# Performance work log

Hardware: AMD Instinct MI355X
Metric: run time of the kernel (lower is better)

The kernel has to match this reference:

```python
import jax, jax.numpy as jnp
import numpy as np

B, H, S, D = 8, 16, 1024, 128


def setup_inputs() -> dict:
    key = jax.random.key(0)
    kq, kk, kv = jax.random.split(key, 3)
    queries = jax.random.normal(kq, (B, H, S, D), dtype=jnp.float32)
    keys = jax.random.normal(kk, (B, H, S, D), dtype=jnp.float32)
    values = jax.random.normal(kv, (B, H, S, D), dtype=jnp.float32)
    # learnable per-element scale over the full score tensor, init 'ones'
    scale = jnp.ones((B, H, S, S), dtype=jnp.float32)
    return {"queries": queries, "keys": keys, "values": values, "scale": scale}


def reference(queries, keys, values, scale):
    # scores: [B,H,Sq,Sk] = Q K^T
    scores = jnp.einsum("bhqd,bhkd->bhqk", queries, keys)
    # custom learnable scaling: scores / sqrt(scale[0]) * scale
    # scale[0] has shape [H,Sq,Sk] and broadcasts over the batch dim
    scores = scores / jnp.sqrt(scale[0]) * scale
    # masked_softmax with attention_mask=None -> plain softmax over keys axis
    attn = jax.nn.softmax(scores, axis=-1)
    # dropout is identity (rate 0 / eval mode)
    out = jnp.einsum("bhqk,bhkd->bhqd", attn, values)
    return out
```

## Files before the change

### kernel.cpp

```cpp
#include <hip/hip_runtime.h>
#include <math.h>

#define NB 8
#define NH 16
#define NS 1024
#define ND 128

#define BN 32
#define NT (NS / BN)
#define TILE_SH (BN * ND)
#define PSTR 40

typedef float    f32x4 __attribute__((ext_vector_type(4)));
typedef _Float16 f16x8 __attribute__((ext_vector_type(8)));
typedef _Float16 f16x4 __attribute__((ext_vector_type(4)));

#define MFMAH(a, b, c) __builtin_amdgcn_mfma_f32_16x16x32_f16(a, b, c, 0, 0, 0)

__device__ __forceinline__ void gload16(const void* g, void* l) {
  __builtin_amdgcn_global_load_lds(
      (const __attribute__((address_space(1))) void*)g,
      (__attribute__((address_space(3))) void*)l, 16, 0, 0);
}

__global__ void prep_kv(const float* __restrict__ K, short* __restrict__ Kimg,
                        const float* __restrict__ V, short* __restrict__ Vimg) {
  __shared__ _Float16 tbuf[BN * 132];
  const int x = blockIdx.x;
  const int tid = threadIdx.x;
  if (x < 4096) {
    const int t = x & 31, bh = x >> 5;
    const float* Kt = K + ((size_t)bh * NS + t * BN) * ND;
    short* img = Kimg + ((size_t)bh * NT + t) * TILE_SH;
#pragma unroll
    for (int i = 0; i < 4; ++i) {
      int f = tid + i * 256;
      int key = f >> 5, d4 = (f & 31) << 2;
      float4 v = *(const float4*)(Kt + (size_t)key * ND + d4);
      f16x4 hv = {(_Float16)v.x, (_Float16)v.y, (_Float16)v.z, (_Float16)v.w};
      int gp = (d4 >> 3) ^ (key & 15);
      *(f16x4*)(img + key * 128 + gp * 8 + (d4 & 7)) = hv;
    }
  } else {
    const int p = x - 4096;
    const int t = p & 31, bh = p >> 5;
    const float* Vt = V + ((size_t)bh * NS + t * BN) * ND;
#pragma unroll
    for (int i = 0; i < 4; ++i) {
      int f = tid + i * 256;
      int key = f >> 5, d4 = (f & 31) << 2;
      float4 v = *(const float4*)(Vt + (size_t)key * ND + d4);
      *(f16x4*)&tbuf[key * 132 + d4] =
          (f16x4){(_Float16)v.x, (_Float16)v.y, (_Float16)v.z, (_Float16)v.w};
    }
    __syncthreads();
    short* img = Vimg + ((size_t)bh * NT + t) * TILE_SH;
#pragma unroll
    for (int i = 0; i < 2; ++i) {
      int u = tid + i * 256;
      int d = u >> 2, k8 = u & 3;
      f16x8 o;
#pragma unroll
      for (int e = 0; e < 8; ++e) o[e] = tbuf[(k8 * 8 + e) * 132 + d];
      *(f16x8*)(img + d * BN + ((k8 ^ ((d >> 1) & 3)) * 8)) = o;
    }
  }
}


#define ISSUE(T, B)                                              \
  do {                                                           \
    const short* kg_ = Kb + (T) * TILE_SH + tid * 8;             \
    const short* vg_ = Vb + (T) * TILE_SH + tid * 8;             \
    gload16(kg_, &Ks[B][tid * 8]);                               \
    gload16(kg_ + 2048, &Ks[B][tid * 8 + 2048]);                 \
    gload16(vg_, &Vs[B][tid * 8]);                               \
    gload16(vg_ + 2048, &Vs[B][tid * 8 + 2048]);                 \
  } while (0)

#define LOADS(SV, S0, T)                                                             \
  do {                                                                               \
    _Pragma("unroll") for (int nf = 0; nf < 2; ++nf)                                 \
        _Pragma("unroll") for (int m0 = 0; m0 < 2; ++m0) {                           \
      size_t off_ = (size_t)(q0 + nf * 16 + c) * NS + (T) * BN + m0 * 16 + quad * 4; \
      SV[nf][m0] = *(const f32x4*)(sclb + off_);                                     \
      S0[nf][m0] = *(const f32x4*)(sc0b + off_);                                     \
    }                                                                                \
  } while (0)

#define TILE_STEP(BUF, SCV, SC0)                                                     \
  do {                                                                               \
    f32x4 S_[2][2];                                                                  \
    _Pragma("unroll") for (int nf = 0; nf < 2; ++nf)                                 \
        _Pragma("unroll") for (int m0 = 0; m0 < 2; ++m0)                             \
            S_[nf][m0] = (f32x4){0.f, 0.f, 0.f, 0.f};                                \
    __builtin_amdgcn_s_setprio(1);                                                   \
    _Pragma("unroll") for (int m0 = 0; m0 < 2; ++m0) {                               \
      _Pragma("unroll") for (int kb = 0; kb < 4; ++kb) {                             \
        const f16x8 a_ = *(const f16x8*)&Ks[BUF][(m0 * 16 + c) * 128 +               \
                                                 (((kb << 2) | quad) ^ c) * 8];      \
        S_[0][m0] = MFMAH(a_, qf[0][kb], S_[0][m0]);                                 \
        S_[1][m0] = MFMAH(a_, qf[1][kb], S_[1][m0]);                                 \
      }                                                                              \
    }                                                                                \
    __builtin_amdgcn_s_setprio(0);                                                   \
    float al2_[2];                                                                   \
    int skipall_ = 1;                                                                \
    _Pragma("unroll") for (int nf = 0; nf < 2; ++nf) {                               \
      float sv[8];                                                                   \
      _Pragma("unroll") for (int m0 = 0; m0 < 2; ++m0)                               \
          _Pragma("unroll") for (int r = 0; r < 4; ++r) {                            \
        float e_ = SCV[nf][m0][r] * rsqrtf(SC0[nf][m0][r]);                          \
        sv[m0 * 4 + r] = S_[nf][m0][r] * e_;                                         \
      }                                                                              \
      float tm = sv[0];                                                              \
      _Pragma("unroll") for (int i = 1; i < 8; ++i) tm = fmaxf(tm, sv[i]);           \
      tm = fmaxf(tm, __shfl_xor(tm, 16));                                            \
      tm = fmaxf(tm, __shfl_xor(tm, 32));                                            \
      float mn, al;                                                                  \
      if (__all(tm <= m_[nf])) {                         \
        mn = m_[nf]; al = 1.f;                                                       \
      } else {                                                                       \
        mn = fmaxf(m_[nf], tm);                                                      \
        al = __expf(m_[nf] - mn);                                                    \
        m_[nf] = mn;                                                                 \
        skipall_ = 0;                                                                \
      }                                                                              \
      al2_[nf] = al;                                                                 \
      float ps = 0.f;                                                                \
      _Float16 pb[8];                                                                \
      _Pragma("unroll") for (int i = 0; i < 8; ++i) {                                \
        float p_ = __expf(sv[i] - mn);                                               \
        ps += p_;                                                                    \
        pb[i] = (_Float16)p_;                                                        \
      }                                                                              \
      ps += __shfl_xor(ps, 16);                                                      \
      ps += __shfl_xor(ps, 32);                                                      \
      ls_[nf] = ls_[nf] * al + ps;                                                   \
      _Float16* pr_ = &Ps[(size_t)(w * 32 + nf * 16 + c) * PSTR];                    \
      *(f16x4*)(pr_ + quad * 4)      = (f16x4){pb[0], pb[1], pb[2], pb[3]};          \
      *(f16x4*)(pr_ + 16 + quad * 4) = (f16x4){pb[4], pb[5], pb[6], pb[7]};          \
    }                                                                                \
    if (!skipall_) {                                                                 \
      _Pragma("unroll") for (int pf = 0; pf < 2; ++pf) {                             \
        float ar_[4];                                                                \
        _Pragma("unroll") for (int r = 0; r < 4; ++r)                                \
            ar_[r] = __shfl(al2_[pf], quad * 4 + r);                                 \
        _Pragma("unroll") for (int n0 = 0; n0 < 8; ++n0)                             \
            _Pragma("unroll") for (int r = 0; r < 4; ++r) O[pf][n0][r] *= ar_[r];    \
      }                                                                              \
    }                                                                                \
    const f16x8 pf0_ = *(const f16x8*)&Ps[(size_t)(w * 32 + c) * PSTR + quad * 8];   \
    const f16x8 pf1_ =                                                               \
        *(const f16x8*)&Ps[(size_t)(w * 32 + 16 + c) * PSTR + quad * 8];             \
    __builtin_amdgcn_s_setprio(1);                                                   \
    _Pragma("unroll") for (int n0 = 0; n0 < 8; ++n0) {                               \
      const f16x8 b_ = *(const f16x8*)&Vs[BUF][(n0 * 16 + c) * 32 +                  \
                                              (quad ^ ((c >> 1) & 3)) * 8];          \
      O[0][n0] = MFMAH(pf0_, b_, O[0][n0]);                                          \
      O[1][n0] = MFMAH(pf1_, b_, O[1][n0]);                                          \
    }                                                                                \
    __builtin_amdgcn_s_setprio(0);                                                   \
  } while (0)

__launch_bounds__(256, 2)
__global__ void attn_f16(const float* __restrict__ Q, const short* __restrict__ Kimg,
                         const short* __restrict__ Vimg, const float* __restrict__ scale,
                         float* __restrict__ out) {
  __shared__ short Ks[2][TILE_SH];
  __shared__ short Vs[2][TILE_SH];
  __shared__ _Float16 Ps[128 * PSTR];

  const int tid = threadIdx.x;
  const int w = tid >> 6, l = tid & 63;
  const int quad = l >> 4, c = l & 15;

  const int x = blockIdx.x;
  const int bh = ((x >> 6) << 3) | (x & 7);
  const int qblk = (x >> 3) & 7;
  const int q0 = qblk * 128 + w * 32;

  const short* Kb = Kimg + (size_t)bh * (NT * TILE_SH);
  const short* Vb = Vimg + (size_t)bh * (NT * TILE_SH);
  const float* sclb = scale + ((size_t)bh << 20);
  const float* sc0b = scale + ((size_t)(bh & 15) << 20);

  f16x8 qf[2][4];
  f32x4 sclvA[2][2], sc0vA[2][2], sclvB[2][2], sc0vB[2][2];
  {
    const float* Qb = Q + ((size_t)bh * NS + q0) * ND;
    float4 qa[2][4][2];
#pragma unroll
    for (int nf = 0; nf < 2; ++nf)
#pragma unroll
      for (int kb = 0; kb < 4; ++kb) {
        const float* p = Qb + (size_t)(nf * 16 + c) * ND + kb * 32 + quad * 8;
        qa[nf][kb][0] = *(const float4*)p;
        qa[nf][kb][1] = *(const float4*)(p + 4);
      }
    ISSUE(0, 0);
    LOADS(sclvA, sc0vA, 0);
#pragma unroll
    for (int nf = 0; nf < 2; ++nf)
#pragma unroll
      for (int kb = 0; kb < 4; ++kb) {
        float4 a = qa[nf][kb][0], b = qa[nf][kb][1];
        qf[nf][kb] = (f16x8){(_Float16)a.x, (_Float16)a.y, (_Float16)a.z, (_Float16)a.w,
                             (_Float16)b.x, (_Float16)b.y, (_Float16)b.z, (_Float16)b.w};
      }
  }

  float m_[2] = {-INFINITY, -INFINITY}, ls_[2] = {0.f, 0.f};
  f32x4 O[2][8];
#pragma unroll
  for (int pf = 0; pf < 2; ++pf)
#pragma unroll
    for (int n0 = 0; n0 < 8; ++n0) O[pf][n0] = (f32x4){0.f, 0.f, 0.f, 0.f};

#pragma unroll 1
  for (int kt = 0; kt < NT; kt += 2) {
    __syncthreads();
    ISSUE(kt + 1, 1);
    LOADS(sclvB, sc0vB, kt + 1);
    TILE_STEP(0, sclvA, sc0vA);
    __syncthreads();
    if (kt + 2 < NT) {
      ISSUE(kt + 2, 0);
      LOADS(sclvA, sc0vA, kt + 2);
    }
    TILE_STEP(1, sclvB, sc0vB);
  }

  float* ob = out + ((size_t)bh * NS + q0) * ND;
#pragma unroll
  for (int pf = 0; pf < 2; ++pf)
#pragma unroll
    for (int r = 0; r < 4; ++r) {
      float lv = __shfl(ls_[pf], quad * 4 + r);
      float inv = 1.0f / lv;
      int row = pf * 16 + quad * 4 + r;
#pragma unroll
      for (int n0 = 0; n0 < 8; ++n0)
        ob[(size_t)row * ND + n0 * 16 + c] = O[pf][n0][r] * inv;
    }
}

#define TQ 16
#define TK 64
#define PITCH 129
__launch_bounds__(256, 2)
__global__ void attn_fp32(const float* __restrict__ Q, const float* __restrict__ K,
                          const float* __restrict__ V, const float* __restrict__ scale,
                          float* __restrict__ out) {
  __shared__ float qs[TQ][ND];
  __shared__ float kv[TK][PITCH];
  __shared__ float ps[4][4][TK];
  const int tid = threadIdx.x;
  const int w = tid >> 6, l = tid & 63;
  const int bid = blockIdx.x;
  const int qt = bid & 63, h = (bid >> 6) & 15, b = bid >> 10;
  const size_t bh = (size_t)b * NH + h;
  const float* Qb = Q + (bh * NS + (size_t)qt * TQ) * ND;
  const float* Kb = K + bh * NS * ND;
  const float* Vb = V + bh * NS * ND;
  {
    const float4* Q4 = (const float4*)Qb;
    float4* qs4 = (float4*)&qs[0][0];
    qs4[tid] = Q4[tid];
    qs4[tid + 256] = Q4[tid + 256];
  }
  const int q0 = qt * TQ + w * 4;
  const float* sc0p[4];
  const float* sclp[4];
#pragma unroll
  for (int i = 0; i < 4; ++i) {
    const int qg = q0 + i;
    sc0p[i] = scale + ((size_t)h * NS + qg) * NS;
    sclp[i] = scale + (bh * NS + qg) * NS;
  }
  float m[4] = {-INFINITY, -INFINITY, -INFINITY, -INFINITY};
  float lsum[4] = {0.f, 0.f, 0.f, 0.f};
  float oa[4] = {0.f, 0.f, 0.f, 0.f};
  float ob[4] = {0.f, 0.f, 0.f, 0.f};
  for (int kt = 0; kt < NS / TK; ++kt) {
    __syncthreads();
    {
      const float4* K4 = (const float4*)(Kb + (size_t)kt * TK * ND);
#pragma unroll
      for (int i = 0; i < 8; ++i) {
        const int f = tid + i * 256;
        const float4 t4 = K4[f];
        const int r = f >> 5, cc = (f & 31) << 2;
        kv[r][cc] = t4.x; kv[r][cc + 1] = t4.y; kv[r][cc + 2] = t4.z; kv[r][cc + 3] = t4.w;
      }
    }
    __syncthreads();
    const int kg = kt * TK + l;
    float sc0[4], scl[4];
#pragma unroll
    for (int i = 0; i < 4; ++i) { sc0[i] = sc0p[i][kg]; scl[i] = sclp[i][kg]; }
    float s[4] = {0.f, 0.f, 0.f, 0.f};
#pragma unroll 8
    for (int d = 0; d < ND; ++d) {
      const float kd = kv[l][d];
      s[0] = fmaf(qs[w * 4 + 0][d], kd, s[0]);
      s[1] = fmaf(qs[w * 4 + 1][d], kd, s[1]);
      s[2] = fmaf(qs[w * 4 + 2][d], kd, s[2]);
      s[3] = fmaf(qs[w * 4 + 3][d], kd, s[3]);
    }
#pragma unroll
    for (int i = 0; i < 4; ++i) {
      const float svv = s[i] * scl[i] * rsqrtf(sc0[i]);
      float mx = svv;
#pragma unroll
      for (int off = 32; off > 0; off >>= 1) mx = fmaxf(mx, __shfl_xor(mx, off));
      const float mn = fmaxf(m[i], mx);
      const float p = __expf(svv - mn);
      const float al = __expf(m[i] - mn);
      float psum = p;
#pragma unroll
      for (int off = 32; off > 0; off >>= 1) psum += __shfl_xor(psum, off);
      lsum[i] = lsum[i] * al + psum;
      m[i] = mn;
      oa[i] *= al;
      ob[i] *= al;
      ps[w][i][l] = p;
    }
    __syncthreads();
    {
      const float4* V4 = (const float4*)(Vb + (size_t)kt * TK * ND);
#pragma unroll
      for (int i = 0; i < 8; ++i) {
        const int f = tid + i * 256;
        const float4 t4 = V4[f];
        const int r = f >> 5, cc = (f & 31) << 2;
        kv[r][cc] = t4.x; kv[r][cc + 1] = t4.y; kv[r][cc + 2] = t4.z; kv[r][cc + 3] = t4.w;
      }
    }
    __syncthreads();
#pragma unroll 4
    for (int k2 = 0; k2 < TK; ++k2) {
      const float v0 = kv[k2][l];
      const float v1 = kv[k2][64 + l];
#pragma unroll
      for (int i = 0; i < 4; ++i) {
        const float p = ps[w][i][k2];
        oa[i] = fmaf(p, v0, oa[i]);
        ob[i] = fmaf(p, v1, ob[i]);
      }
    }
  }
  float* op = out + (bh * NS + q0) * ND;
#pragma unroll
  for (int i = 0; i < 4; ++i) {
    const float inv = 1.0f / lsum[i];
    op[(size_t)i * ND + l] = oa[i] * inv;
    op[(size_t)i * ND + 64 + l] = ob[i] * inv;
  }
}

extern "C" void kernel_launch(void* const* d_in, const int* in_sizes, int n_in,
                              void* d_out, int out_size, void* d_ws, size_t ws_size,
                              hipStream_t stream) {
  const float* Q = (const float*)d_in[0];
  const float* K = (const float*)d_in[1];
  const float* V = (const float*)d_in[2];
  const float* scale = (const float*)d_in[3];
  float* out = (float*)d_out;

  const size_t KV_BYTES = (size_t)NB * NH * NS * ND * 2;
  const size_t needB = 2 * KV_BYTES;

  if (ws_size >= needB) {
    short* Kimg = (short*)d_ws;
    short* Vimg = (short*)((char*)d_ws + KV_BYTES);
    prep_kv<<<dim3(8192), dim3(256), 0, stream>>>(K, Kimg, V, Vimg);
    attn_f16<<<dim3(1024), dim3(256), 0, stream>>>(Q, Kimg, Vimg, scale, out);
  } else {
    attn_fp32<<<dim3(NB * NH * (NS / TK) * 4), dim3(256), 0, stream>>>(Q, K, V, scale,
                                                                       out);
  }
}
```

Baseline: 932.9 us.

## Precompute fp16 effective score scale in prep kernel and stream via LDS

The prep kernel gains a third block range. It computes scale*rsqrt(scale[0]) once per element and writes it as an fp16 tiled image into the workspace. A new attention kernel loads these tiles into shared memory with async global-to-LDS copies, prefetching the next tile after a barrier. This removes the per-tile fp32 loads of both scale tensors and the rsqrt from the main loop, and raises launch bounds to 3 blocks per CU. In exchange it adds an extra full pass over the scale tensor, a large workspace requirement, an extra barrier per tile, and fp16 rounding of the scale factor.

```diff
diff --git a/kernel.cpp b/kernel.cpp
--- a/kernel.cpp
+++ b/kernel.cpp
@@ -9,6 +9,7 @@
 #define BN 32
 #define NT (NS / BN)
 #define TILE_SH (BN * ND)
+#define ETILE (128 * BN)
 #define PSTR 40
 
 typedef float    f32x4 __attribute__((ext_vector_type(4)));
@@ -23,8 +24,9 @@
       (__attribute__((address_space(3))) void*)l, 16, 0, 0);
 }
 
-__global__ void prep_kv(const float* __restrict__ K, short* __restrict__ Kimg,
-                        const float* __restrict__ V, short* __restrict__ Vimg) {
+__global__ void prep_all(const float* __restrict__ K, short* __restrict__ Kimg,
+                         const float* __restrict__ V, short* __restrict__ Vimg,
+                         const float* __restrict__ scale, _Float16* __restrict__ Eimg) {
   __shared__ _Float16 tbuf[BN * 132];
   const int x = blockIdx.x;
   const int tid = threadIdx.x;
@@ -41,7 +43,7 @@
       int gp = (d4 >> 3) ^ (key & 15);
       *(f16x4*)(img + key * 128 + gp * 8 + (d4 & 7)) = hv;
     }
-  } else {
+  } else if (x < 8192) {
     const int p = x - 4096;
     const int t = p & 31, bh = p >> 5;
     const float* Vt = V + ((size_t)bh * NS + t * BN) * ND;
@@ -63,6 +65,56 @@
 #pragma unroll
       for (int e = 0; e < 8; ++e) o[e] = tbuf[(k8 * 8 + e) * 132 + d];
       *(f16x8*)(img + d * BN + ((k8 ^ ((d >> 1) & 3)) * 8)) = o;
+    }
+  } else {
+    const int p = x - 8192;
+    const int qg = p & 7, t = (p >> 3) & 31, h = p >> 8;
+    const int q = qg * 128 + (tid >> 1);
+    const int kh = (tid & 1) * 16;
+    const int qloc = tid >> 1;
+    const float* s0p = scale + ((size_t)h << 20) + (size_t)q * NS + t * 32 + kh;
+    float4 s0[4];
+#pragma unroll
+    for (int i = 0; i < 4; ++i) s0[i] = *(const float4*)(s0p + i * 4);
+    float rs[16];
+#pragma unroll
+    for (int i = 0; i < 4; ++i) {
+      rs[i * 4 + 0] = rsqrtf(s0[i].x);
+      rs[i * 4 + 1] = rsqrtf(s0[i].y);
+      rs[i * 4 + 2] = rsqrtf(s0[i].z);
+      rs[i * 4 + 3] = rsqrtf(s0[i].w);
+    }
+    {
+      _Float16* ep = Eimg + (((size_t)h * 8 + qg) * NT + t) * ETILE + qloc * 32 + kh;
+      f16x8 o0, o1;
+#pragma unroll
+      for (int j = 0; j < 4; ++j) {
+        o0[j] = (_Float16)(s0[0][j] * rs[j]);
+        o0[4 + j] = (_Float16)(s0[1][j] * rs[4 + j]);
+        o1[j] = (_Float16)(s0[2][j] * rs[8 + j]);
+        o1[4 + j] = (_Float16)(s0[3][j] * rs[12 + j]);
+      }
+      *(f16x8*)ep = o0;
+      *(f16x8*)(ep + 8) = o1;
+    }
+#pragma unroll
+    for (int b = 1; b < NB; ++b) {
+      const int bh = b * NH + h;
+      const float* slp = scale + ((size_t)bh << 20) + (size_t)q * NS + t * 32 + kh;
+      float4 sl[4];
+#pragma unroll
+      for (int i = 0; i < 4; ++i) sl[i] = *(const float4*)(slp + i * 4);
+      _Float16* ep = Eimg + (((size_t)bh * 8 + qg) * NT + t) * ETILE + qloc * 32 + kh;
+      f16x8 o0, o1;
+#pragma unroll
+      for (int j = 0; j < 4; ++j) {
+        o0[j] = (_Float16)(sl[0][j] * rs[j]);
+        o0[4 + j] = (_Float16)(sl[1][j] * rs[4 + j]);
+        o1[j] = (_Float16)(sl[2][j] * rs[8 + j]);
+        o1[4 + j] = (_Float16)(sl[3][j] * rs[12 + j]);
+      }
+      *(f16x8*)ep = o0;
+      *(f16x8*)(ep + 8) = o1;
     }
   }
 }
@@ -78,17 +130,14 @@
     gload16(vg_ + 2048, &Vs[B][tid * 8 + 2048]);                 \
   } while (0)
 
-#define LOADS(SV, S0, T)                                                             \
-  do {                                                                               \
-    _Pragma("unroll") for (int nf = 0; nf < 2; ++nf)                                 \
-        _Pragma("unroll") for (int m0 = 0; m0 < 2; ++m0) {                           \
-      size_t off_ = (size_t)(q0 + nf * 16 + c) * NS + (T) * BN + m0 * 16 + quad * 4; \
-      SV[nf][m0] = *(const f32x4*)(sclb + off_);                                     \
-      S0[nf][m0] = *(const f32x4*)(sc0b + off_);                                     \
-    }                                                                                \
+#define ISSUE_E(T)                                               \
+  do {                                                           \
+    const _Float16* eg_ = Eb + (size_t)(T) * ETILE + tid * 8;    \
+    gload16(eg_, &Es[tid * 8]);                                  \
+    gload16(eg_ + 2048, &Es[tid * 8 + 2048]);                    \
   } while (0)
 
-#define TILE_STEP(BUF, SCV, SC0)                                                     \
+#define TILE_STEP_E(BUF, T)                                                          \
   do {                                                                               \
     f32x4 S_[2][2];                                                                  \
     _Pragma("unroll") for (int nf = 0; nf < 2; ++nf)                                 \
@@ -108,10 +157,11 @@
     int skipall_ = 1;                                                                \
     _Pragma("unroll") for (int nf = 0; nf < 2; ++nf) {                               \
       float sv[8];                                                                   \
-      _Pragma("unroll") for (int m0 = 0; m0 < 2; ++m0)                               \
-          _Pragma("unroll") for (int r = 0; r < 4; ++r) {                            \
-        float e_ = SCV[nf][m0][r] * rsqrtf(SC0[nf][m0][r]);                          \
-        sv[m0 * 4 + r] = S_[nf][m0][r] * e_;                                         \
+      _Pragma("unroll") for (int m0 = 0; m0 < 2; ++m0) {                             \
+        const f16x4 ef_ =                                                            \
+            *(const f16x4*)&Es[(w * 32 + nf * 16 + c) * 32 + m0 * 16 + quad * 4];    \
+        _Pragma("unroll") for (int r = 0; r < 4; ++r)                                \
+            sv[m0 * 4 + r] = S_[nf][m0][r] * (float)ef_[r];                          \
       }                                                                              \
       float tm = sv[0];                                                              \
       _Pragma("unroll") for (int i = 1; i < 8; ++i) tm = fmaxf(tm, sv[i]);           \
@@ -150,6 +200,11 @@
             _Pragma("unroll") for (int r = 0; r < 4; ++r) O[pf][n0][r] *= ar_[r];    \
       }                                                                              \
     }                                                                                \
+        \
+                                       \
+    asm volatile("s_waitcnt lgkmcnt(0)" ::: "memory");                               \
+    __builtin_amdgcn_s_barrier();                                                    \
+    if ((T) + 1 < NT) ISSUE_E((T) + 1);                                              \
     const f16x8 pf0_ = *(const f16x8*)&Ps[(size_t)(w * 32 + c) * PSTR + quad * 8];   \
     const f16x8 pf1_ =                                                               \
         *(const f16x8*)&Ps[(size_t)(w * 32 + 16 + c) * PSTR + quad * 8];             \
@@ -163,6 +218,164 @@
     __builtin_amdgcn_s_setprio(0);                                                   \
   } while (0)
 
+__launch_bounds__(256, 3)
+__global__ void attn_f16_e(const float* __restrict__ Q, const short* __restrict__ Kimg,
+                           const short* __restrict__ Vimg,
+                           const _Float16* __restrict__ Eimg, float* __restrict__ out) {
+  __shared__ short Ks[2][TILE_SH];
+  __shared__ short Vs[2][TILE_SH];
+  __shared__ _Float16 Es[ETILE];
+  __shared__ _Float16 Ps[128 * PSTR];
+
+  const int tid = threadIdx.x;
+  const int w = tid >> 6, l = tid & 63;
+  const int quad = l >> 4, c = l & 15;
+
+  const int x = blockIdx.x;
+  const int bh = ((x >> 6) << 3) | (x & 7);
+  const int qblk = (x >> 3) & 7;
+  const int q0 = qblk * 128 + w * 32;
+
+  const short* Kb = Kimg + (size_t)bh * (NT * TILE_SH);
+  const short* Vb = Vimg + (size_t)bh * (NT * TILE_SH);
+  const _Float16* Eb = Eimg + ((size_t)bh * 8 + qblk) * (NT * ETILE);
+
+  f16x8 qf[2][4];
+  {
+    const float* Qb = Q + ((size_t)bh * NS + q0) * ND;
+    float4 qa[2][4][2];
+#pragma unroll
+    for (int nf = 0; nf < 2; ++nf)
+#pragma unroll
+      for (int kb = 0; kb < 4; ++kb) {
+        const float* p = Qb + (size_t)(nf * 16 + c) * ND + kb * 32 + quad * 8;
+        qa[nf][kb][0] = *(const float4*)p;
+        qa[nf][kb][1] = *(const float4*)(p + 4);
+      }
+    ISSUE(0, 0);
+    ISSUE_E(0);
+#pragma unroll
+    for (int nf = 0; nf < 2; ++nf)
+#pragma unroll
+      for (int kb = 0; kb < 4; ++kb) {
+        float4 a = qa[nf][kb][0], b = qa[nf][kb][1];
+        qf[nf][kb] = (f16x8){(_Float16)a.x, (_Float16)a.y, (_Float16)a.z, (_Float16)a.w,
+                             (_Float16)b.x, (_Float16)b.y, (_Float16)b.z, (_Float16)b.w};
+      }
+  }
+
+  float m_[2] = {-INFINITY, -INFINITY}, ls_[2] = {0.f, 0.f};
+  f32x4 O[2][8];
+#pragma unroll
+  for (int pf = 0; pf < 2; ++pf)
+#pragma unroll
+    for (int n0 = 0; n0 < 8; ++n0) O[pf][n0] = (f32x4){0.f, 0.f, 0.f, 0.f};
+
+#pragma unroll 1
+  for (int kt = 0; kt < NT; kt += 2) {
+    __syncthreads();
+    ISSUE(kt + 1, 1);
+    TILE_STEP_E(0, kt);
+    __syncthreads();
+    if (kt + 2 < NT) ISSUE(kt + 2, 0);
+    TILE_STEP_E(1, kt + 1);
+  }
+
+  float* ob = out + ((size_t)bh * NS + q0) * ND;
+#pragma unroll
+  for (int pf = 0; pf < 2; ++pf)
+#pragma unroll
+    for (int r = 0; r < 4; ++r) {
+      float lv = __shfl(ls_[pf], quad * 4 + r);
+      float inv = 1.0f / lv;
+      int row = pf * 16 + quad * 4 + r;
+#pragma unroll
+      for (int n0 = 0; n0 < 8; ++n0)
+        ob[(size_t)row * ND + n0 * 16 + c] = O[pf][n0][r] * inv;
+    }
+}
+
+#define LOADS(SV, S0, T)                                                             \
+  do {                                                                               \
+    _Pragma("unroll") for (int nf = 0; nf < 2; ++nf)                                 \
+        _Pragma("unroll") for (int m0 = 0; m0 < 2; ++m0) {                           \
+      size_t off_ = (size_t)(q0 + nf * 16 + c) * NS + (T) * BN + m0 * 16 + quad * 4; \
+      SV[nf][m0] = *(const f32x4*)(sclb + off_);                                     \
+      S0[nf][m0] = *(const f32x4*)(sc0b + off_);                                     \
+    }                                                                                \
+  } while (0)
+
+#define TILE_STEP(BUF, SCV, SC0)                                                     \
+  do {                                                                               \
+    f32x4 S_[2][2];                                                                  \
+    _Pragma("unroll") for (int nf = 0; nf < 2; ++nf)                                 \
+        _Pragma("unroll") for (int m0 = 0; m0 < 2; ++m0)                             \
+            S_[nf][m0] = (f32x4){0.f, 0.f, 0.f, 0.f};                                \
+    _Pragma("unroll") for (int m0 = 0; m0 < 2; ++m0) {                               \
+      _Pragma("unroll") for (int kb = 0; kb < 4; ++kb) {                             \
+        const f16x8 a_ = *(const f16x8*)&Ks[BUF][(m0 * 16 + c) * 128 +               \
+                                                 (((kb << 2) | quad) ^ c) * 8];      \
+        S_[0][m0] = MFMAH(a_, qf[0][kb], S_[0][m0]);                                 \
+        S_[1][m0] = MFMAH(a_, qf[1][kb], S_[1][m0]);                                 \
+      }                                                                              \
+    }                                                                                \
+    float al2_[2];                                                                   \
+    int skipall_ = 1;                                                                \
+    _Pragma("unroll") for (int nf = 0; nf < 2; ++nf) {                               \
+      float sv[8];                                                                   \
+      _Pragma("unroll") for (int m0 = 0; m0 < 2; ++m0)                               \
+          _Pragma("unroll") for (int r = 0; r < 4; ++r) {                            \
+        float e_ = SCV[nf][m0][r] * rsqrtf(SC0[nf][m0][r]);                          \
+        sv[m0 * 4 + r] = S_[nf][m0][r] * e_;                                         \
+      }                                                                              \
+      float tm = sv[0];                                                              \
+      _Pragma("unroll") for (int i = 1; i < 8; ++i) tm = fmaxf(tm, sv[i]);           \
+      tm = fmaxf(tm, __shfl_xor(tm, 16));                                            \
+      tm = fmaxf(tm, __shfl_xor(tm, 32));                                            \
+      float mn, al;                                                                  \
+      if (__all(tm <= m_[nf])) {                                                     \
+        mn = m_[nf]; al = 1.f;                                                       \
+      } else {                                                                       \
+        mn = fmaxf(m_[nf], tm);                                                      \
+        al = __expf(m_[nf] - mn);                                                    \
+        m_[nf] = mn;                                                                 \
+        skipall_ = 0;                                                                \
+      }                                                                              \
+      al2_[nf] = al;                                                                 \
+      float ps = 0.f;                                                                \
+      _Float16 pb[8];                                                                \
+      _Pragma("unroll") for (int i = 0; i < 8; ++i) {                                \
+        float p_ = __expf(sv[i] - mn);                                               \
+        ps += p_;                                                                    \
+        pb[i] = (_Float16)p_;                                                        \
+      }                                                                              \
+      ps += __shfl_xor(ps, 16);                                                      \
+      ps += __shfl_xor(ps, 32);                                                      \
+      ls_[nf] = ls_[nf] * al + ps;                                                   \
+      _Float16* pr_ = &Ps[(size_t)(w * 32 + nf * 16 + c) * PSTR];                    \
+      *(f16x4*)(pr_ + quad * 4)      = (f16x4){pb[0], pb[1], pb[2], pb[3]};          \
+      *(f16x4*)(pr_ + 16 + quad * 4) = (f16x4){pb[4], pb[5], pb[6], pb[7]};          \
+    }                                                                                \
+    if (!skipall_) {                                                                 \
+      _Pragma("unroll") for (int pf = 0; pf < 2; ++pf) {                             \
+        float ar_[4];                                                                \
+        _Pragma("unroll") for (int r = 0; r < 4; ++r)                                \
+            ar_[r] = __shfl(al2_[pf], quad * 4 + r);                                 \
+        _Pragma("unroll") for (int n0 = 0; n0 < 8; ++n0)                             \
+            _Pragma("unroll") for (int r = 0; r < 4; ++r) O[pf][n0][r] *= ar_[r];    \
+      }                                                                              \
+    }                                                                                \
+    const f16x8 pf0_ = *(const f16x8*)&Ps[(size_t)(w * 32 + c) * PSTR + quad * 8];   \
+    const f16x8 pf1_ =                                                               \
+        *(const f16x8*)&Ps[(size_t)(w * 32 + 16 + c) * PSTR + quad * 8];             \
+    _Pragma("unroll") for (int n0 = 0; n0 < 8; ++n0) {                               \
+      const f16x8 b_ = *(const f16x8*)&Vs[BUF][(n0 * 16 + c) * 32 +                  \
+                                              (quad ^ ((c >> 1) & 3)) * 8];          \
+      O[0][n0] = MFMAH(pf0_, b_, O[0][n0]);                                          \
+      O[1][n0] = MFMAH(pf1_, b_, O[1][n0]);                                          \
+    }                                                                                \
+  } while (0)
+
 __launch_bounds__(256, 2)
 __global__ void attn_f16(const float* __restrict__ Q, const short* __restrict__ Kimg,
                          const short* __restrict__ Vimg, const float* __restrict__ scale,
@@ -174,7 +387,6 @@
   const int tid = threadIdx.x;
   const int w = tid >> 6, l = tid & 63;
   const int quad = l >> 4, c = l & 15;
-
   const int x = blockIdx.x;
   const int bh = ((x >> 6) << 3) | (x & 7);
   const int qblk = (x >> 3) & 7;
@@ -369,12 +581,20 @@
   float* out = (float*)d_out;
 
   const size_t KV_BYTES = (size_t)NB * NH * NS * ND * 2;
+  const size_t E_BYTES = (size_t)NB * NH * NS * NS * 2;
   const size_t needB = 2 * KV_BYTES;
-
-  if (ws_size >= needB) {
+  const size_t needA = needB + E_BYTES;
+
+  if (ws_size >= needA) {
     short* Kimg = (short*)d_ws;
     short* Vimg = (short*)((char*)d_ws + KV_BYTES);
-    prep_kv<<<dim3(8192), dim3(256), 0, stream>>>(K, Kimg, V, Vimg);
+    _Float16* Eimg = (_Float16*)((char*)d_ws + needB);
+    prep_all<<<dim3(12288), dim3(256), 0, stream>>>(K, Kimg, V, Vimg, scale, Eimg);
+    attn_f16_e<<<dim3(1024), dim3(256), 0, stream>>>(Q, Kimg, Vimg, Eimg, out);
+  } else if (ws_size >= needB) {
+    short* Kimg = (short*)d_ws;
+    short* Vimg = (short*)((char*)d_ws + KV_BYTES);
+    prep_all<<<dim3(8192), dim3(256), 0, stream>>>(K, Kimg, V, Vimg, nullptr, nullptr);
     attn_f16<<<dim3(1024), dim3(256), 0, stream>>>(Q, Kimg, Vimg, scale, out);
   } else {
     attn_fp32<<<dim3(NB * NH * (NS / TK) * 4), dim3(256), 0, stream>>>(Q, K, V, scale,
```

New measurement: 1.044 ms. +11.9%, slower.
